# Kernel optimization log

Measured on AMD Instinct MI355X. Metric: run time of the kernel, lower is better.

The kernel has to match this reference:

```python
import jax, jax.numpy as jnp
import numpy as np
from jax import lax

D_MODEL = 1024
D_STATE = 16
EXPAND = 2
KERNEL = 4
BATCH = 4
SEQ = 4096
LN_EPS = 1e-5


def _ln(x, w, b):
    m = jnp.mean(x, axis=-1, keepdims=True)
    v = jnp.mean((x - m) ** 2, axis=-1, keepdims=True)
    return (x - m) * lax.rsqrt(v + LN_EPS) * w + b


def setup_inputs() -> dict:
    key = jax.random.key(0)
    ks = jax.random.split(key, 16)
    d, n, e, k = D_MODEL, D_STATE, EXPAND, KERNEL

    def lin(key, fan_in, shape):
        bound = 1.0 / np.sqrt(fan_in)
        return jax.random.uniform(key, shape, jnp.float32, -bound, bound)

    return {
        "x": jax.random.normal(ks[0], (BATCH, SEQ, d), jnp.float32),
        "ln1_w": jnp.ones((d,), jnp.float32),
        "ln1_b": jnp.zeros((d,), jnp.float32),
        "conv_w": lin(ks[1], k, (d, 1, k)),  # depthwise conv, groups=d -> fan_in=k
        "conv_b": lin(ks[2], k, (d,)),
        "lns_w": jnp.ones((d,), jnp.float32),
        "lns_b": jnp.zeros((d,), jnp.float32),
        "in_w": lin(ks[3], d, (d, 2 * d)),
        "in_b": lin(ks[4], d, (2 * d,)),
        "xp_w": lin(ks[5], d, (d, n)),
        "xp_b": lin(ks[6], d, (n,)),
        "A_log": jax.random.normal(ks[7], (n,), jnp.float32),
        "D": jax.random.normal(ks[8], (n, d), jnp.float32),
        "out_w": lin(ks[9], d, (d, d)),
        "out_b": lin(ks[10], d, (d,)),
        "ln2_w": jnp.ones((d,), jnp.float32),
        "ln2_b": jnp.zeros((d,), jnp.float32),
        "mlp_w1": lin(ks[11], d, (d, e * d)),
        "mlp_b1": lin(ks[12], d, (e * d,)),
        "mlp_w2": lin(ks[13], e * d, (e * d, d)),
        "mlp_b2": lin(ks[14], e * d, (d,)),
    }


def reference(x, ln1_w, ln1_b, conv_w, conv_b, lns_w, lns_b, in_w, in_b,
              xp_w, xp_b, A_log, D, out_w, out_b, ln2_w, ln2_b,
              mlp_w1, mlp_b1, mlp_w2, mlp_b2):
    b, s, d = x.shape
    # --- depthwise causal-padded conv branch (truncated to seq_len) ---
    xn = _ln(x, ln1_w, ln1_b)
    xc = jnp.transpose(xn, (0, 2, 1))  # (b, d, s)
    xc = lax.conv_general_dilated(
        xc, conv_w, window_strides=(1,), padding=[(KERNEL - 1, KERNEL - 1)],
        feature_group_count=d, dimension_numbers=("NCH", "OIH", "NCH"))
    xc = xc + conv_b[None, :, None]
    xc = jnp.transpose(xc, (0, 2, 1))[:, :s]  # (b, s, d)
    x = x + xc

    # --- SelectiveScanLayer ---
    residual = x
    xn = _ln(x, lns_w, lns_b)
    xz = xn @ in_w + in_b
    xp, z = jnp.split(xz, 2, axis=-1)
    xp = jax.nn.silu(xp)
    z = jax.nn.sigmoid(z)
    u = xp @ xp_w + xp_b  # (b, s, n)
    decay = jnp.exp(-jnp.exp(A_log))  # exp(A), A = -exp(A_log); (n,)

    u_t = jnp.transpose(u, (1, 0, 2))  # (s, b, n)

    def step(h, u_i):
        h = decay * h + u_i
        return h, h

    _, hs = lax.scan(step, jnp.zeros((b, D_STATE), x.dtype), u_t)  # (s, b, n)
    ys = jnp.einsum("sbn,nd->sbd", hs, D) * jnp.transpose(z, (1, 0, 2))
    ys = ys @ out_w + out_b  # (s, b, d)
    # faithful to original: torch stack gives (1,s,b,d), then .view(b,s,d)
    y = ys.reshape(b, s, d)
    x = residual + y

    # --- MLP (dropout inactive at eval) ---
    h = _ln(x, ln2_w, ln2_b)
    h = jax.nn.gelu(h @ mlp_w1 + mlp_b1, approximate=False)
    h = h @ mlp_w2 + mlp_b2
    return x + h
```

## Files before the change

### kernel.cpp

```cpp
#include <hip/hip_runtime.h>
#include <cstdint>
#include <cstddef>


typedef short bf16x8 __attribute__((ext_vector_type(8)));
typedef float f32x4 __attribute__((ext_vector_type(4)));

#define GLD16(gp, lp)                                                          \
  __builtin_amdgcn_global_load_lds(                                            \
      (__attribute__((address_space(1))) void*)(gp),                           \
      (__attribute__((address_space(3))) void*)(lp), 16, 0, 0)

static __device__ __forceinline__ ushort f2bf(float f) {
  union { float f; uint32_t u; } c; c.f = f;
  uint32_t r = c.u + 0x7FFFu + ((c.u >> 16) & 1u);
  return (ushort)(r >> 16);
}
static __device__ __forceinline__ float bf2f(ushort u) {
  union { uint32_t u; float f; } c; c.u = ((uint32_t)u) << 16;
  return c.f;
}

template <int BF16OUT>
__global__ __launch_bounds__(256) void ln_kernel(
    const float* __restrict__ x, const float* __restrict__ w,
    const float* __restrict__ b, void* __restrict__ out) {
  const int row = blockIdx.x;
  const int tid = threadIdx.x;
  const float4 v = ((const float4*)(x + (size_t)row * 1024))[tid];
  float s  = v.x + v.y + v.z + v.w;
  float s2 = v.x * v.x + v.y * v.y + v.z * v.z + v.w * v.w;
#pragma unroll
  for (int off = 32; off > 0; off >>= 1) {
    s  += __shfl_down(s, off);
    s2 += __shfl_down(s2, off);
  }
  __shared__ float red[8];
  const int wv = tid >> 6, ln = tid & 63;
  if (ln == 0) { red[wv] = s; red[4 + wv] = s2; }
  __syncthreads();
  s  = red[0] + red[1] + red[2] + red[3];
  s2 = red[4] + red[5] + red[6] + red[7];
  const float mean = s * (1.f / 1024.f);
  const float var  = s2 * (1.f / 1024.f) - mean * mean;
  const float rstd = rsqrtf(var + 1e-5f);
  const float4 wv4 = ((const float4*)w)[tid];
  const float4 bv4 = ((const float4*)b)[tid];
  const float o0 = (v.x - mean) * rstd * wv4.x + bv4.x;
  const float o1 = (v.y - mean) * rstd * wv4.y + bv4.y;
  const float o2 = (v.z - mean) * rstd * wv4.z + bv4.z;
  const float o3 = (v.w - mean) * rstd * wv4.w + bv4.w;
  if (BF16OUT) {
    ushort4 o; o.x = f2bf(o0); o.y = f2bf(o1); o.z = f2bf(o2); o.w = f2bf(o3);
    ((ushort4*)((ushort*)out + (size_t)row * 1024))[tid] = o;
  } else {
    float4 o; o.x = o0; o.y = o1; o.z = o2; o.w = o3;
    ((float4*)((float*)out + (size_t)row * 1024))[tid] = o;
  }
}

__global__ __launch_bounds__(256) void lnconv_kernel(
    const float* __restrict__ x, const float* __restrict__ ln1w,
    const float* __restrict__ ln1b, const float* __restrict__ cw,
    const float* __restrict__ cb, const float* __restrict__ lnsw,
    const float* __restrict__ lnsb, float* __restrict__ x1,
    ushort* __restrict__ abuf) {
  const int row = blockIdx.x;
  const int t = row & 4095;
  const int tid = threadIdx.x;
  const int wv = tid >> 6, ln = tid & 63;
  const float4* x4 = (const float4*)x;
  float4 xr[4];
  float s[4], q[4];
#pragma unroll
  for (int j = 0; j < 4; j++) {
    const int tt = t - 3 + j;
    if (tt >= 0)
      xr[j] = x4[(size_t)(row - 3 + j) * 256 + tid];
    else
      xr[j] = make_float4(0.f, 0.f, 0.f, 0.f);
    s[j] = xr[j].x + xr[j].y + xr[j].z + xr[j].w;
    q[j] = xr[j].x * xr[j].x + xr[j].y * xr[j].y + xr[j].z * xr[j].z +
           xr[j].w * xr[j].w;
  }
#pragma unroll
  for (int off = 32; off > 0; off >>= 1) {
#pragma unroll
    for (int j = 0; j < 4; j++) {
      s[j] += __shfl_down(s[j], off);
      q[j] += __shfl_down(q[j], off);
    }
  }
  __shared__ float red[4][8];
  __shared__ float red2[8];
  if (ln == 0) {
#pragma unroll
    for (int j = 0; j < 4; j++) { red[wv][j] = s[j]; red[wv][4 + j] = q[j]; }
  }
  __syncthreads();
  float4 wv4 = ((const float4*)ln1w)[tid];
  float4 bv4 = ((const float4*)ln1b)[tid];
  const int c0 = tid * 4;
  float4 acc = *(const float4*)(cb + c0);
  const float4 w0 = *(const float4*)(cw + (size_t)(c0 + 0) * 4);
  const float4 w1 = *(const float4*)(cw + (size_t)(c0 + 1) * 4);
  const float4 w2 = *(const float4*)(cw + (size_t)(c0 + 2) * 4);
  const float4 w3 = *(const float4*)(cw + (size_t)(c0 + 3) * 4);
#pragma unroll
  for (int j = 0; j < 4; j++) {
    if (t - 3 + j >= 0) {
      const float sm = red[0][j] + red[1][j] + red[2][j] + red[3][j];
      const float sq = red[0][4 + j] + red[1][4 + j] + red[2][4 + j] +
                       red[3][4 + j];
      const float mean = sm * (1.f / 1024.f);
      const float var  = sq * (1.f / 1024.f) - mean * mean;
      const float rstd = rsqrtf(var + 1e-5f);
      const float lx = (xr[j].x - mean) * rstd * wv4.x + bv4.x;
      const float ly = (xr[j].y - mean) * rstd * wv4.y + bv4.y;
      const float lz = (xr[j].z - mean) * rstd * wv4.z + bv4.z;
      const float lw = (xr[j].w - mean) * rstd * wv4.w + bv4.w;
      acc.x += lx * ((const float*)&w0)[j];
      acc.y += ly * ((const float*)&w1)[j];
      acc.z += lz * ((const float*)&w2)[j];
      acc.w += lw * ((const float*)&w3)[j];
    }
  }
  float4 o;
  o.x = xr[3].x + acc.x; o.y = xr[3].y + acc.y;
  o.z = xr[3].z + acc.z; o.w = xr[3].w + acc.w;
  ((float4*)x1)[(size_t)row * 256 + tid] = o;
  float s2 = o.x + o.y + o.z + o.w;
  float q2 = o.x * o.x + o.y * o.y + o.z * o.z + o.w * o.w;
#pragma unroll
  for (int off = 32; off > 0; off >>= 1) {
    s2 += __shfl_down(s2, off);
    q2 += __shfl_down(q2, off);
  }
  if (ln == 0) { red2[wv] = s2; red2[4 + wv] = q2; }
  __syncthreads();
  const float sm = red2[0] + red2[1] + red2[2] + red2[3];
  const float sq = red2[4] + red2[5] + red2[6] + red2[7];
  const float mean = sm * (1.f / 1024.f);
  const float var  = sq * (1.f / 1024.f) - mean * mean;
  const float rstd = rsqrtf(var + 1e-5f);
  wv4 = ((const float4*)lnsw)[tid];
  bv4 = ((const float4*)lnsb)[tid];
  ushort4 a;
  a.x = f2bf((o.x - mean) * rstd * wv4.x + bv4.x);
  a.y = f2bf((o.y - mean) * rstd * wv4.y + bv4.y);
  a.z = f2bf((o.z - mean) * rstd * wv4.z + bv4.z);
  a.w = f2bf((o.w - mean) * rstd * wv4.w + bv4.w);
  ((ushort4*)(abuf + (size_t)row * 1024))[tid] = a;
}

__global__ __launch_bounds__(256) void wt_all_kernel(
    const float* __restrict__ in_w, const float* __restrict__ out_w,
    const float* __restrict__ w1, const float* __restrict__ w2,
    ushort* __restrict__ in_wT, ushort* __restrict__ out_wT,
    ushort* __restrict__ w1T, ushort* __restrict__ w2T) {
  __shared__ float tile[32][33];
  const int idx = blockIdx.x;
  const float* src; ushort* dst; int K, N, n0, k0;
  if (idx < 2048) {
    src = in_w; dst = in_wT; K = 1024; N = 2048;
    n0 = (idx & 63) * 32; k0 = (idx >> 6) * 32;
  } else if (idx < 3072) {
    const int r = idx - 2048;
    src = out_w; dst = out_wT; K = 1024; N = 1024;
    n0 = (r & 31) * 32; k0 = (r >> 5) * 32;
  } else if (idx < 5120) {
    const int r = idx - 3072;
    src = w1; dst = w1T; K = 1024; N = 2048;
    n0 = (r & 63) * 32; k0 = (r >> 6) * 32;
  } else {
    const int r = idx - 5120;
    src = w2; dst = w2T; K = 2048; N = 1024;
    n0 = (r & 31) * 32; k0 = (r >> 5) * 32;
  }
  const int tx = threadIdx.x & 31, ty = threadIdx.x >> 5;
#pragma unroll
  for (int j = 0; j < 32; j += 8)
    tile[ty + j][tx] = src[(size_t)(k0 + ty + j) * N + n0 + tx];
  __syncthreads();
#pragma unroll
  for (int j = 0; j < 32; j += 8)
    dst[(size_t)(n0 + ty + j) * K + k0 + tx] = f2bf(tile[tx][ty + j]);
}

__global__ __launch_bounds__(256) void u_mfma_kernel(
    const ushort* __restrict__ xp, const float* __restrict__ xpw,
    const float* __restrict__ xpb, float* __restrict__ u) {
  __shared__ ushort Ws[16 * 1024];
  __shared__ ushort As[64 * 64];
  const int tid = threadIdx.x;
  const int wave = tid >> 6, lane = tid & 63;
  const int l16 = lane & 15, quad = lane >> 4;
  for (int e = tid; e < 16384; e += 256) {
    const int n = e & 15, k = e >> 4;
    Ws[n * 1024 + (((k >> 3) ^ (n & 7)) << 3) + (k & 7)] =
        f2bf(xpw[(size_t)k * 16 + n]);
  }
  const int bm0 = blockIdx.x * 64;
  const int srow = lane >> 3, sblk = (lane & 7) ^ (srow & 7);
  const ushort* Ag = xp + (size_t)(bm0 + wave * 16 + srow) * 1024 + sblk * 8;
  ushort* Al = &As[wave * 16 * 64];
  const int rsw = l16 & 7;
  f32x4 acc = (f32x4){0.f, 0.f, 0.f, 0.f};
  __syncthreads();
  for (int k0 = 0; k0 < 1024; k0 += 64) {
    GLD16(Ag + k0, Al);
    GLD16(Ag + k0 + (size_t)8 * 1024, Al + 512);
    __syncthreads();
#pragma unroll
    for (int kh = 0; kh < 2; kh++) {
      const bf16x8 aF = *(const bf16x8*)
          &As[(wave * 16 + l16) * 64 + (((kh * 4 + quad) ^ rsw) << 3)];
      const bf16x8 bF = *(const bf16x8*)
          &Ws[l16 * 1024 + ((((k0 >> 3) + kh * 4 + quad) ^ rsw) << 3)];
      acc = __builtin_amdgcn_mfma_f32_16x16x32_bf16(aF, bF, acc, 0, 0, 0);
    }
    __syncthreads();
  }
  const float bv = xpb[l16];
#pragma unroll
  for (int r = 0; r < 4; r++) {
    const int row = bm0 + wave * 16 + quad * 4 + r;
    u[(size_t)row * 16 + l16] = acc[r] + bv;
  }
}

__global__ __launch_bounds__(256) void scan_kernel(
    const float* __restrict__ u, const float* __restrict__ A_log,
    float* __restrict__ hs) {
  const int tid = threadIdx.x;
  const int b = blockIdx.x >> 4;
  const int n = blockIdx.x & 15;
  const float d = expf(-expf(A_log[n]));
  const int t0 = tid * 16;
  const float* up = u + ((size_t)b * 4096) * 16 + n;
  float loc[16];
  float h = 0.f;
#pragma unroll
  for (int i = 0; i < 16; i++) {
    h = d * h + up[(size_t)(t0 + i) * 16];
    loc[i] = h;
  }
  __shared__ float sv[256];
  sv[tid] = h;
  __syncthreads();
  float d16 = d * d; d16 *= d16; d16 *= d16; d16 *= d16;
  float f = d16;
  for (int off = 1; off < 256; off <<= 1) {
    const float add = (tid >= off) ? sv[tid - off] : 0.f;
    __syncthreads();
    sv[tid] += f * add;
    __syncthreads();
    f *= f;
  }
  const float carry = (tid > 0) ? sv[tid - 1] : 0.f;
  float dp = d;
#pragma unroll
  for (int i = 0; i < 16; i++) {
    const float hg = loc[i] + dp * carry;
    dp *= d;
    hs[((size_t)(t0 + i) * 4 + b) * 16 + n] = hg;
  }
}

__global__ __launch_bounds__(256) void g_kernel(
    const float* __restrict__ hs, const float* __restrict__ Dm,
    const ushort* __restrict__ z, ushort* __restrict__ g) {
  __shared__ float hsh[256];
  const int tid = threadIdx.x;
  const int r0 = blockIdx.x * 16;
  hsh[tid] = hs[(size_t)r0 * 16 + tid];
  __syncthreads();
  float4 acc[16];
#pragma unroll
  for (int rr = 0; rr < 16; rr++) acc[rr] = make_float4(0.f, 0.f, 0.f, 0.f);
  const float4* Dv = (const float4*)Dm;
#pragma unroll
  for (int n = 0; n < 16; n++) {
    const float4 dv = Dv[(size_t)n * 256 + tid];
#pragma unroll
    for (int rr = 0; rr < 16; rr++) {
      const float h = hsh[rr * 16 + n];
      acc[rr].x += h * dv.x; acc[rr].y += h * dv.y;
      acc[rr].z += h * dv.z; acc[rr].w += h * dv.w;
    }
  }
#pragma unroll
  for (int rr = 0; rr < 16; rr++) {
    const int r = r0 + rr;
    const int b = r & 3, t = r >> 2;
    const ushort4 zv =
        *(const ushort4*)(z + ((size_t)b * 4096 + t) * 1024 + tid * 4);
    ushort4 o;
    o.x = f2bf(acc[rr].x * bf2f(zv.x)); o.y = f2bf(acc[rr].y * bf2f(zv.y));
    o.z = f2bf(acc[rr].z * bf2f(zv.z)); o.w = f2bf(acc[rr].w * bf2f(zv.w));
    *(ushort4*)(g + (size_t)r * 1024 + tid * 4) = o;
  }
}

template <int EPI>
__global__ __launch_bounds__(256) void gemm_bt(
    const ushort* __restrict__ A, const ushort* __restrict__ Bt,
    const float* __restrict__ bias, int K, void* __restrict__ p0,
    void* __restrict__ p1) {
  __shared__ ushort As[128 * 64];
  __shared__ ushort Bs[128 * 64];
  const int tid = threadIdx.x;
  const int wave = tid >> 6, lane = tid & 63;
  const int l16 = lane & 15, quad = lane >> 4;
  const int bm0 = blockIdx.x * 128, bn0 = blockIdx.y * 128;
  const int wr = (wave >> 1) * 64, wc = (wave & 1) * 64;
  const int srow = lane >> 3;
  const int sblk = (lane & 7) ^ (srow & 7);

  const ushort* Ag = A + (size_t)(bm0 + wave * 32 + srow) * K + sblk * 8;
  const ushort* Bg = Bt + (size_t)(bn0 + wave * 32 + srow) * K + sblk * 8;
  ushort* Al = &As[wave * 32 * 64];
  ushort* Bl = &Bs[wave * 32 * 64];
  const int rsw = l16 & 7;

  f32x4 acc[4][4];
#pragma unroll
  for (int i = 0; i < 4; i++)
#pragma unroll
    for (int j = 0; j < 4; j++) acc[i][j] = (f32x4){0.f, 0.f, 0.f, 0.f};

  for (int k0 = 0; k0 < K; k0 += 64) {
#pragma unroll
    for (int i = 0; i < 4; i++) {
      GLD16(Ag + (size_t)(i * 8) * K + k0, Al + i * 512);
      GLD16(Bg + (size_t)(i * 8) * K + k0, Bl + i * 512);
    }
    __syncthreads();
#pragma unroll
    for (int kh = 0; kh < 2; kh++) {
      const int c8 = ((kh * 4 + quad) ^ rsw) << 3;
      bf16x8 aF[4], bF[4];
#pragma unroll
      for (int i = 0; i < 4; i++)
        aF[i] = *(const bf16x8*)&As[(wr + i * 16 + l16) * 64 + c8];
#pragma unroll
      for (int j = 0; j < 4; j++)
        bF[j] = *(const bf16x8*)&Bs[(wc + j * 16 + l16) * 64 + c8];
#pragma unroll
      for (int i = 0; i < 4; i++)
#pragma unroll
        for (int j = 0; j < 4; j++)
          acc[i][j] = __builtin_amdgcn_mfma_f32_16x16x32_bf16(
              aF[i], bF[j], acc[i][j], 0, 0, 0);
    }
    __syncthreads();
  }

#pragma unroll
  for (int i = 0; i < 4; i++) {
    const int row0 = bm0 + wr + i * 16 + quad * 4;
#pragma unroll
    for (int j = 0; j < 4; j++) {
      const int c = bn0 + wc + j * 16 + l16;
      const float bv = bias[c];
#pragma unroll
      for (int r = 0; r < 4; r++) {
        const size_t row = (size_t)(row0 + r);
        const float v = acc[i][j][r] + bv;
        if (EPI == 0) {
          if (c < 1024)
            ((ushort*)p0)[row * 1024 + c] = f2bf(v / (1.f + __expf(-v)));
          else
            ((ushort*)p1)[row * 1024 + (c - 1024)] =
                f2bf(1.f / (1.f + __expf(-v)));
        } else if (EPI == 1) {
          float* io = (float*)p0;
          io[row * 1024 + c] += v;
        } else if (EPI == 2) {
          ((ushort*)p0)[row * 2048 + c] =
              f2bf(0.5f * v * (1.f + erff(v * 0.70710678118654752f)));
        } else {
          ((float*)p0)[row * 1024 + c] =
              ((const float*)p1)[row * 1024 + c] + v;
        }
      }
    }
  }
}

extern "C" void kernel_launch(void* const* d_in, const int* in_sizes, int n_in,
                              void* d_out, int out_size, void* d_ws,
                              size_t ws_size, hipStream_t stream) {
  const float* x      = (const float*)d_in[0];
  const float* ln1_w  = (const float*)d_in[1];
  const float* ln1_b  = (const float*)d_in[2];
  const float* conv_w = (const float*)d_in[3];
  const float* conv_b = (const float*)d_in[4];
  const float* lns_w  = (const float*)d_in[5];
  const float* lns_b  = (const float*)d_in[6];
  const float* in_w   = (const float*)d_in[7];
  const float* in_b   = (const float*)d_in[8];
  const float* xp_w   = (const float*)d_in[9];
  const float* xp_b   = (const float*)d_in[10];
  const float* A_log  = (const float*)d_in[11];
  const float* Dm     = (const float*)d_in[12];
  const float* out_w  = (const float*)d_in[13];
  const float* out_b  = (const float*)d_in[14];
  const float* ln2_w  = (const float*)d_in[15];
  const float* ln2_b  = (const float*)d_in[16];
  const float* mlp_w1 = (const float*)d_in[17];
  const float* mlp_b1 = (const float*)d_in[18];
  const float* mlp_w2 = (const float*)d_in[19];
  const float* mlp_b2 = (const float*)d_in[20];

  char* wsp = (char*)d_ws;
  size_t off = 0;
  auto alloc = [&](size_t bytes) {
    void* p = wsp + off;
    off += (bytes + 255) & ~(size_t)255;
    return p;
  };
  float*  x1    = (float*)alloc(67108864);
  ushort* abuf  = (ushort*)alloc(67108864);
  ushort* gbuf  = abuf + 16777216;
  ushort* xpb   = (ushort*)alloc(33554432);
  ushort* zb    = (ushort*)alloc(67108864);
  ushort* h1b   = (ushort*)zb;
  float*  ub    = (float*)alloc(1048576);
  float*  hsb   = (float*)alloc(1048576);
  ushort* in_wT = (ushort*)alloc(4194304);
  ushort* out_wT= (ushort*)alloc(2097152);
  ushort* w1T   = (ushort*)alloc(4194304);
  ushort* w2T   = (ushort*)alloc(4194304);

  wt_all_kernel<<<7168, 256, 0, stream>>>(in_w, out_w, mlp_w1, mlp_w2,
                                          in_wT, out_wT, w1T, w2T);
  lnconv_kernel<<<16384, 256, 0, stream>>>(x, ln1_w, ln1_b, conv_w, conv_b,
                                           lns_w, lns_b, x1, abuf);
  gemm_bt<0><<<dim3(128, 16), 256, 0, stream>>>(abuf, in_wT, in_b, 1024,
                                                xpb, zb);
  u_mfma_kernel<<<256, 256, 0, stream>>>(xpb, xp_w, xp_b, ub);
  scan_kernel<<<64, 256, 0, stream>>>(ub, A_log, hsb);
  g_kernel<<<1024, 256, 0, stream>>>(hsb, Dm, zb, gbuf);
  gemm_bt<1><<<dim3(128, 8), 256, 0, stream>>>(gbuf, out_wT, out_b, 1024,
                                               x1, nullptr);
  ln_kernel<1><<<16384, 256, 0, stream>>>(x1, ln2_w, ln2_b, xpb);
  gemm_bt<2><<<dim3(128, 16), 256, 0, stream>>>(xpb, w1T, mlp_b1, 1024,
                                                h1b, nullptr);
  gemm_bt<3><<<dim3(128, 8), 256, 0, stream>>>(h1b, w2T, mlp_b2, 2048,
                                               d_out, x1);
}
```

Baseline: 691.1 us.

## Rewrite GEMM as 256x256 tile, 8-wave, double-buffered pipelined kernel with XCD swizzle

Replaces the 128x128 single-buffered GEMM with a 256x256 tile computed by 512 threads (8 waves), using a 128 KB double-buffered LDS region. Global-to-LDS loads for the next k-tile are interleaved between four MFMA phases, with explicit barriers, waitcnts and setprio. Block indices are remapped so that consecutive blocks on the same XCD share A rows for L2 reuse. The goal is to hide memory latency and raise MFMA utilisation. In exchange it uses more LDS and registers per block and lowers the block count, which can hurt occupancy and tail balance.

```diff
diff --git a/kernel.cpp b/kernel.cpp
--- a/kernel.cpp
+++ b/kernel.cpp
@@ -303,65 +303,168 @@
 }
 
 template <int EPI>
-__global__ __launch_bounds__(256) void gemm_bt(
+__global__ __launch_bounds__(512, 2) void gemm_bt(
     const ushort* __restrict__ A, const ushort* __restrict__ Bt,
     const float* __restrict__ bias, int K, void* __restrict__ p0,
     void* __restrict__ p1) {
-  __shared__ ushort As[128 * 64];
-  __shared__ ushort Bs[128 * 64];
+  __shared__ __align__(16) ushort sm[65536];
   const int tid = threadIdx.x;
   const int wave = tid >> 6, lane = tid & 63;
   const int l16 = lane & 15, quad = lane >> 4;
-  const int bm0 = blockIdx.x * 128, bn0 = blockIdx.y * 128;
-  const int wr = (wave >> 1) * 64, wc = (wave & 1) * 64;
+  const int wm = wave >> 2, wn = wave & 3;
+
+  const int nbx = (int)gridDim.x;
+  int tm, tn;
+  if ((nbx & 7) == 0) {
+    const int lid = (int)blockIdx.y * nbx + (int)blockIdx.x;
+    const int ncm = nbx >> 3;
+    const int xcd = lid & 7;
+    const int j = lid >> 3;
+    tm = xcd * ncm + (j % ncm);
+    tn = j / ncm;
+  } else {
+    tm = (int)blockIdx.x; tn = (int)blockIdx.y;
+  }
+  const int bm0 = tm * 256, bn0 = tn * 256;
+
   const int srow = lane >> 3;
-  const int sblk = (lane & 7) ^ (srow & 7);
-
-  const ushort* Ag = A + (size_t)(bm0 + wave * 32 + srow) * K + sblk * 8;
-  const ushort* Bg = Bt + (size_t)(bn0 + wave * 32 + srow) * K + sblk * 8;
-  ushort* Al = &As[wave * 32 * 64];
-  ushort* Bl = &Bs[wave * 32 * 64];
+  const int sblk = (lane & 7) ^ srow;
+  const int NT = K >> 6;
+
+  const ushort* Astg = A + (size_t)(bm0 + wave * 8 + srow) * K + sblk * 8;
+  const ushort* Bstg = Bt + (size_t)(bn0 + wave * 8 + srow) * K + sblk * 8;
+
+#define SA(i, kt, base)                                                        \
+  GLD16(Astg + (size_t)((i) * 64) * K + (kt) * 64,                             \
+        &sm[(base) + (i) * 4096 + wave * 512])
+#define SB(i, kt, base)                                                        \
+  GLD16(Bstg + (size_t)((i) * 64) * K + (kt) * 64,                             \
+        &sm[(base) + 16384 + (i) * 4096 + wave * 512])
+
   const int rsw = l16 & 7;
-
-  f32x4 acc[4][4];
-#pragma unroll
-  for (int i = 0; i < 4; i++)
+  const int c80 = (quad ^ rsw) << 3;
+  const int c81 = ((4 + quad) ^ rsw) << 3;
+  const int aoff = (wm * 128 + l16) * 64;
+  const int boff = 16384 + (wn * 64 + l16) * 64;
+
+  f32x4 acc[8][4];
+#pragma unroll
+  for (int i = 0; i < 8; i++)
 #pragma unroll
     for (int j = 0; j < 4; j++) acc[i][j] = (f32x4){0.f, 0.f, 0.f, 0.f};
 
-  for (int k0 = 0; k0 < K; k0 += 64) {
+  SA(0, 0, 0); SA(1, 0, 0); SA(2, 0, 0); SA(3, 0, 0);
+  SB(0, 0, 0); SB(1, 0, 0); SB(2, 0, 0); SB(3, 0, 0);
+  if (NT > 1) {
+    SA(0, 1, 32768); SA(1, 1, 32768);
+    asm volatile("s_waitcnt vmcnt(2)" ::: "memory");
+  } else {
+    asm volatile("s_waitcnt vmcnt(0)" ::: "memory");
+  }
+  __builtin_amdgcn_s_barrier();
+
+  bf16x8 af[4][2], b01[2][2], b23[2][2];
+
+  for (int t = 0; t < NT; ++t) {
+    const int cb = (t & 1) << 15;
+    const int nb = cb ^ 32768;
 #pragma unroll
     for (int i = 0; i < 4; i++) {
-      GLD16(Ag + (size_t)(i * 8) * K + k0, Al + i * 512);
-      GLD16(Bg + (size_t)(i * 8) * K + k0, Bl + i * 512);
-    }
-    __syncthreads();
-#pragma unroll
-    for (int kh = 0; kh < 2; kh++) {
-      const int c8 = ((kh * 4 + quad) ^ rsw) << 3;
-      bf16x8 aF[4], bF[4];
-#pragma unroll
-      for (int i = 0; i < 4; i++)
-        aF[i] = *(const bf16x8*)&As[(wr + i * 16 + l16) * 64 + c8];
-#pragma unroll
-      for (int j = 0; j < 4; j++)
-        bF[j] = *(const bf16x8*)&Bs[(wc + j * 16 + l16) * 64 + c8];
-#pragma unroll
-      for (int i = 0; i < 4; i++)
-#pragma unroll
-        for (int j = 0; j < 4; j++)
-          acc[i][j] = __builtin_amdgcn_mfma_f32_16x16x32_bf16(
-              aF[i], bF[j], acc[i][j], 0, 0, 0);
-    }
-    __syncthreads();
-  }
-
-#pragma unroll
-  for (int i = 0; i < 4; i++) {
-    const int row0 = bm0 + wr + i * 16 + quad * 4;
+      af[i][0] = *(const bf16x8*)&sm[cb + aoff + i * 1024 + c80];
+      af[i][1] = *(const bf16x8*)&sm[cb + aoff + i * 1024 + c81];
+    }
+#pragma unroll
+    for (int j = 0; j < 2; j++) {
+      b01[j][0] = *(const bf16x8*)&sm[cb + boff + j * 1024 + c80];
+      b01[j][1] = *(const bf16x8*)&sm[cb + boff + j * 1024 + c81];
+    }
+    if (t + 1 < NT) { SA(2, t + 1, nb); SA(3, t + 1, nb); }
+    __builtin_amdgcn_s_barrier();
+    asm volatile("s_waitcnt lgkmcnt(0)" ::: "memory");
+    __builtin_amdgcn_sched_barrier(0);
+    __builtin_amdgcn_s_setprio(1);
+#pragma unroll
+    for (int i = 0; i < 4; i++)
+#pragma unroll
+      for (int j = 0; j < 2; j++) {
+        acc[i][j] = __builtin_amdgcn_mfma_f32_16x16x32_bf16(
+            af[i][0], b01[j][0], acc[i][j], 0, 0, 0);
+        acc[i][j] = __builtin_amdgcn_mfma_f32_16x16x32_bf16(
+            af[i][1], b01[j][1], acc[i][j], 0, 0, 0);
+      }
+    __builtin_amdgcn_s_setprio(0);
+    __builtin_amdgcn_s_barrier();
+#pragma unroll
+    for (int j = 0; j < 2; j++) {
+      b23[j][0] = *(const bf16x8*)&sm[cb + boff + (2 + j) * 1024 + c80];
+      b23[j][1] = *(const bf16x8*)&sm[cb + boff + (2 + j) * 1024 + c81];
+    }
+    if (t + 1 < NT) { SB(0, t + 1, nb); SB(1, t + 1, nb); }
+    __builtin_amdgcn_s_barrier();
+    asm volatile("s_waitcnt lgkmcnt(0)" ::: "memory");
+    __builtin_amdgcn_sched_barrier(0);
+    __builtin_amdgcn_s_setprio(1);
+#pragma unroll
+    for (int i = 0; i < 4; i++)
+#pragma unroll
+      for (int j = 0; j < 2; j++) {
+        acc[i][2 + j] = __builtin_amdgcn_mfma_f32_16x16x32_bf16(
+            af[i][0], b23[j][0], acc[i][2 + j], 0, 0, 0);
+        acc[i][2 + j] = __builtin_amdgcn_mfma_f32_16x16x32_bf16(
+            af[i][1], b23[j][1], acc[i][2 + j], 0, 0, 0);
+      }
+    __builtin_amdgcn_s_setprio(0);
+    __builtin_amdgcn_s_barrier();
+#pragma unroll
+    for (int i = 0; i < 4; i++) {
+      af[i][0] = *(const bf16x8*)&sm[cb + aoff + (4 + i) * 1024 + c80];
+      af[i][1] = *(const bf16x8*)&sm[cb + aoff + (4 + i) * 1024 + c81];
+    }
+    if (t + 1 < NT) { SB(2, t + 1, nb); SB(3, t + 1, nb); }
+    __builtin_amdgcn_s_barrier();
+    asm volatile("s_waitcnt lgkmcnt(0)" ::: "memory");
+    __builtin_amdgcn_sched_barrier(0);
+    __builtin_amdgcn_s_setprio(1);
+#pragma unroll
+    for (int i = 0; i < 4; i++)
+#pragma unroll
+      for (int j = 0; j < 2; j++) {
+        acc[4 + i][j] = __builtin_amdgcn_mfma_f32_16x16x32_bf16(
+            af[i][0], b01[j][0], acc[4 + i][j], 0, 0, 0);
+        acc[4 + i][j] = __builtin_amdgcn_mfma_f32_16x16x32_bf16(
+            af[i][1], b01[j][1], acc[4 + i][j], 0, 0, 0);
+      }
+    __builtin_amdgcn_s_setprio(0);
+    __builtin_amdgcn_s_barrier();
+    if (t + 2 < NT) { SA(0, t + 2, cb); SA(1, t + 2, cb); }
+    __builtin_amdgcn_s_barrier();
+    __builtin_amdgcn_s_setprio(1);
+#pragma unroll
+    for (int i = 0; i < 4; i++)
+#pragma unroll
+      for (int j = 0; j < 2; j++) {
+        acc[4 + i][2 + j] = __builtin_amdgcn_mfma_f32_16x16x32_bf16(
+            af[i][0], b23[j][0], acc[4 + i][2 + j], 0, 0, 0);
+        acc[4 + i][2 + j] = __builtin_amdgcn_mfma_f32_16x16x32_bf16(
+            af[i][1], b23[j][1], acc[4 + i][2 + j], 0, 0, 0);
+      }
+    __builtin_amdgcn_s_setprio(0);
+    if (t + 2 < NT) {
+      asm volatile("s_waitcnt vmcnt(2)" ::: "memory");
+    } else {
+      asm volatile("s_waitcnt vmcnt(0)" ::: "memory");
+    }
+    __builtin_amdgcn_s_barrier();
+  }
+#undef SA
+#undef SB
+
+#pragma unroll
+  for (int i = 0; i < 8; i++) {
+    const int row0 = bm0 + wm * 128 + i * 16 + quad * 4;
 #pragma unroll
     for (int j = 0; j < 4; j++) {
-      const int c = bn0 + wc + j * 16 + l16;
+      const int c = bn0 + wn * 64 + j * 16 + l16;
       const float bv = bias[c];
 #pragma unroll
       for (int r = 0; r < 4; r++) {
@@ -437,16 +540,16 @@
                                           in_wT, out_wT, w1T, w2T);
   lnconv_kernel<<<16384, 256, 0, stream>>>(x, ln1_w, ln1_b, conv_w, conv_b,
                                            lns_w, lns_b, x1, abuf);
-  gemm_bt<0><<<dim3(128, 16), 256, 0, stream>>>(abuf, in_wT, in_b, 1024,
-                                                xpb, zb);
+  gemm_bt<0><<<dim3(64, 8), 512, 0, stream>>>(abuf, in_wT, in_b, 1024,
+                                              xpb, zb);
   u_mfma_kernel<<<256, 256, 0, stream>>>(xpb, xp_w, xp_b, ub);
   scan_kernel<<<64, 256, 0, stream>>>(ub, A_log, hsb);
   g_kernel<<<1024, 256, 0, stream>>>(hsb, Dm, zb, gbuf);
-  gemm_bt<1><<<dim3(128, 8), 256, 0, stream>>>(gbuf, out_wT, out_b, 1024,
-                                               x1, nullptr);
+  gemm_bt<1><<<dim3(64, 4), 512, 0, stream>>>(gbuf, out_wT, out_b, 1024,
+                                              x1, nullptr);
   ln_kernel<1><<<16384, 256, 0, stream>>>(x1, ln2_w, ln2_b, xpb);
-  gemm_bt<2><<<dim3(128, 16), 256, 0, stream>>>(xpb, w1T, mlp_b1, 1024,
-                                                h1b, nullptr);
-  gemm_bt<3><<<dim3(128, 8), 256, 0, stream>>>(h1b, w2T, mlp_b2, 2048,
-                                               d_out, x1);
-}
+  gemm_bt<2><<<dim3(64, 8), 512, 0, stream>>>(xpb, w1T, mlp_b1, 1024,
+                                              h1b, nullptr);
+  gemm_bt<3><<<dim3(64, 4), 512, 0, stream>>>(h1b, w2T, mlp_b2, 2048,
+                                              d_out, x1);
+}
```

Result: faster. 618.9 us (-10.5%).
